# Performance work log

Hardware: AMD Instinct MI355X
Metric: run time of the kernel (lower is better)

## Reference

```python
import jax, jax.numpy as jnp
import numpy as np
import math

D_MODEL = 1024
NUM_HEADS = 16
D_K = D_MODEL // NUM_HEADS
B, L = 2, 2048
ROPE_BASE = 10000.0


def _rope_cos_sin(seq_len, dim, dtype=jnp.float32):
    inv_freq = 1.0 / (ROPE_BASE ** (jnp.arange(0, dim, 2, dtype=jnp.float32) / dim))
    t = jnp.arange(seq_len, dtype=jnp.float32)
    freqs = jnp.outer(t, inv_freq)            # [L, dim/2]
    emb = jnp.concatenate([freqs, freqs], -1)  # [L, dim]
    return jnp.cos(emb).astype(dtype), jnp.sin(emb).astype(dtype)


def _apply_rope(x, cos, sin):
    # x: [B, H, L, d_k]; cos/sin: [L, d_k]
    x1, x2 = jnp.split(x, 2, axis=-1)
    rotated = jnp.concatenate([-x2, x1], axis=-1)
    return x * cos + rotated * sin


def setup_inputs() -> dict:
    key = jax.random.key(0)
    ks = jax.random.split(key, 12)
    s = 1.0 / math.sqrt(D_MODEL)
    inp = {
        "query": jax.random.normal(ks[0], (B, L, D_MODEL), jnp.float32),
        "key":   jax.random.normal(ks[1], (B, L, D_MODEL), jnp.float32),
        "value": jax.random.normal(ks[2], (B, L, D_MODEL), jnp.float32),
        "mask":  jnp.triu(jnp.ones((L, L), jnp.bool_), k=1)[None, None],  # causal, True = masked
        "Wq": jax.random.uniform(ks[3], (D_MODEL, D_MODEL), jnp.float32, -s, s),
        "bq": jnp.zeros((D_MODEL,), jnp.float32),
        "Wk": jax.random.uniform(ks[4], (D_MODEL, D_MODEL), jnp.float32, -s, s),
        "bk": jnp.zeros((D_MODEL,), jnp.float32),
        "Wv": jax.random.uniform(ks[5], (D_MODEL, D_MODEL), jnp.float32, -s, s),
        "bv": jnp.zeros((D_MODEL,), jnp.float32),
        "Wo": jax.random.uniform(ks[6], (D_MODEL, D_MODEL), jnp.float32, -s, s),
        "bo": jnp.zeros((D_MODEL,), jnp.float32),
    }
    return inp


def reference(query, key, value, mask, Wq, bq, Wk, bk, Wv, bv, Wo, bo):
    b, l, _ = query.shape
    def proj(x, W, bias):
        return (x @ W.T + bias).reshape(b, l, NUM_HEADS, D_K).transpose(0, 2, 1, 3)
    q = proj(query, Wq, bq)   # [B, H, L, d_k]
    k = proj(key,   Wk, bk)
    v = proj(value, Wv, bv)
    cos, sin = _rope_cos_sin(l, D_K, q.dtype)
    q = _apply_rope(q, cos, sin)
    k = _apply_rope(k, cos, sin)
    scale = 1.0 / math.sqrt(D_K)
    att = jnp.einsum('bhqd,bhkd->bhqk', q, k) * scale
    att = jnp.where(mask, jnp.finfo(att.dtype).min, att)
    att = jax.nn.softmax(att, axis=-1)
    out = jnp.einsum('bhqk,bhkd->bhqd', att, v)
    out = out.transpose(0, 2, 1, 3).reshape(b, l, D_MODEL)
    return out @ Wo.T + bo
```

## Files before the change

kernel.cpp:

```cpp
#include <hip/hip_runtime.h>
#include <cstdint>

typedef _Float16 half_t;
using half8 = __attribute__((ext_vector_type(8))) half_t;
using half4 = __attribute__((ext_vector_type(4))) half_t;
using f32x4 = __attribute__((ext_vector_type(4))) float;
using f32x16 = __attribute__((ext_vector_type(16))) float;

#define LSEQ 2048
#define DM   1024
#define NH   16
#define DK   64

__device__ inline void gload_lds16(const void* g, void* l) {
    __builtin_amdgcn_global_load_lds(
        (const __attribute__((address_space(1))) uint32_t*)g,
        (__attribute__((address_space(3))) uint32_t*)l, 16, 0, 0);
}

__device__ inline uint32_t pk2(float a, float b) {
    auto h = __builtin_amdgcn_cvt_pkrtz(a, b);
    return __builtin_bit_cast(uint32_t, h);
}

__device__ inline float ex2(float x) { return __builtin_amdgcn_exp2f(x); }

__global__ __launch_bounds__(256) void cvt_kernel(
    const float* __restrict__ q, const float* __restrict__ k, const float* __restrict__ v,
    const float* __restrict__ wq, const float* __restrict__ wk,
    const float* __restrict__ wv, const float* __restrict__ wo,
    half_t* __restrict__ dst)
{
    long tid = (long)blockIdx.x * 256 + threadIdx.x;
    long e = tid * 4;
    const float* src;
    long off;
    if (e < 12582912L) {
        int a = (int)(e >> 22);
        src = (a == 0) ? q : (a == 1) ? k : v;
        off = e & 4194303L;
    } else {
        long ew = e - 12582912L;
        int w = (int)(ew >> 20);
        src = (w == 0) ? wq : (w == 1) ? wk : (w == 2) ? wv : wo;
        off = ew & 1048575L;
    }
    float4 x = *(const float4*)(src + off);
    half4 o;
    o[0] = (half_t)x.x; o[1] = (half_t)x.y; o[2] = (half_t)x.z; o[3] = (half_t)x.w;
    *(half4*)(dst + e) = o;
}

__global__ __launch_bounds__(256) void rope_tab(float* __restrict__ cosT, float* __restrict__ sinT) {
    int tid = blockIdx.x * 256 + threadIdx.x;
    int pos = tid >> 5;
    int j = tid & 31;
    float invf = powf(10000.0f, -(float)j / 32.0f);
    float a = (float)pos * invf;
    cosT[tid] = cosf(a);
    sinT[tid] = sinf(a);
}

__global__ __launch_bounds__(256) void qkv_gemm(
    const half_t* __restrict__ XH, const half_t* __restrict__ WH,
    const float* __restrict__ bq, const float* __restrict__ bk, const float* __restrict__ bv,
    half_t* __restrict__ QF, half_t* __restrict__ KF, half_t* __restrict__ VF,
    const float* __restrict__ cosT, const float* __restrict__ sinT)
{
    __shared__ alignas(16) unsigned short sA[128 * 32];
    __shared__ alignas(16) unsigned short sB[128 * 32];
    const int mode = blockIdx.z;
    const half_t* A  = XH + (long)mode * 4194304L;
    const half_t* Bw = WH + (long)mode * 1048576L;
    const float* bias = (mode == 0) ? bq : (mode == 1) ? bk : bv;

    const int tid = threadIdx.x;
    const int lane = tid & 63, wid = tid >> 6;
    const int g = lane >> 4, c = lane & 15;
    const int wr = wid >> 1, wc = wid & 1;
    const int row0 = blockIdx.y * 128, col0 = blockIdx.x * 128;

    f32x4 acc[4][4] = {};
    const int srow = lane >> 2;
    const int scol = (lane & 3) * 8;

    for (int k0 = 0; k0 < DM; k0 += 32) {
#pragma unroll
        for (int i = 0; i < 2; ++i) {
            int r = i * 64 + wid * 16;
            gload_lds16(A  + (long)(row0 + r + srow) * DM + k0 + scol, &sA[r * 32]);
            gload_lds16(Bw + (long)(col0 + r + srow) * DM + k0 + scol, &sB[r * 32]);
        }
        __syncthreads();
        half8 af[4], bf[4];
#pragma unroll
        for (int m = 0; m < 4; ++m)
            af[m] = *(const half8*)&sA[(wr * 64 + m * 16 + c) * 32 + g * 8];
#pragma unroll
        for (int n = 0; n < 4; ++n)
            bf[n] = *(const half8*)&sB[(wc * 64 + n * 16 + c) * 32 + g * 8];
#pragma unroll
        for (int m = 0; m < 4; ++m)
#pragma unroll
            for (int n = 0; n < 4; ++n)
                acc[m][n] = __builtin_amdgcn_mfma_f32_16x16x32_f16(af[m], bf[n], acc[m][n], 0, 0, 0);
        __syncthreads();
    }

    if (mode == 2) {
        const int h = blockIdx.x * 2 + wc;
#pragma unroll
        for (int n = 0; n < 4; ++n) {
            int col = col0 + wc * 64 + n * 16 + c;
            int d = n * 16 + c;
            float bvv = bias[col];
#pragma unroll
            for (int m = 0; m < 4; ++m)
#pragma unroll
                for (int r = 0; r < 4; ++r) {
                    int row = row0 + wr * 64 + m * 16 + g * 4 + r;
                    int b = row >> 11, pos = row & 2047;
                    int bh = b * NH + h;
                    long idx = (((((long)bh * 32 + (pos >> 6)) * 2 + (d >> 5)) * 4
                                 + ((pos >> 4) & 3)) * 64
                                + (((pos >> 3) & 1) * 32 + (d & 31))) * 8 + (pos & 7);
                    VF[idx] = (half_t)(acc[m][n][r] + bvv);
                }
        }
    } else {
        const float SC = (mode == 0) ? 0.125f * 1.44269504f : 1.0f;
        half_t* OF = (mode == 0) ? QF : KF;
#pragma unroll
        for (int np = 0; np < 2; ++np) {
            int col1 = col0 + wc * 64 + np * 16 + c;
            int h = col1 >> 6;
            int d1 = np * 16 + c;
            float b1 = bias[col1], b2 = bias[col1 + 32];
#pragma unroll
            for (int m = 0; m < 4; ++m)
#pragma unroll
                for (int r = 0; r < 4; ++r) {
                    int row = row0 + wr * 64 + m * 16 + g * 4 + r;
                    int b = row >> 11, pos = row & 2047;
                    int bh = b * NH + h;
                    float cv = cosT[pos * 32 + d1], sv = sinT[pos * 32 + d1];
                    float x1 = acc[m][np][r] + b1;
                    float x2 = acc[m][np + 2][r] + b2;
                    long kbase = ((long)(bh * 64 + (pos >> 5)) * 4) * 512
                               + ((c >> 3) * 32 + (pos & 31)) * 8 + (c & 7);
                    OF[kbase + (long)np * 512]       = (half_t)((x1 * cv - x2 * sv) * SC);
                    OF[kbase + (long)(np + 2) * 512] = (half_t)((x2 * cv + x1 * sv) * SC);
                }
        }
    }
}

__global__ __launch_bounds__(256) void out_gemm(
    const half_t* __restrict__ A, const half_t* __restrict__ Bw,
    const float* __restrict__ bias, float* __restrict__ o32)
{
    __shared__ alignas(16) unsigned short sA[128 * 32];
    __shared__ alignas(16) unsigned short sB[128 * 32];
    const int tid = threadIdx.x;
    const int lane = tid & 63, wid = tid >> 6;
    const int g = lane >> 4, c = lane & 15;
    const int wr = wid >> 1, wc = wid & 1;
    const int row0 = blockIdx.y * 128, col0 = blockIdx.x * 128;

    f32x4 acc[4][4] = {};
    const int srow = lane >> 2;
    const int scol = (lane & 3) * 8;

    for (int k0 = 0; k0 < DM; k0 += 32) {
#pragma unroll
        for (int i = 0; i < 2; ++i) {
            int r = i * 64 + wid * 16;
            gload_lds16(A  + (long)(row0 + r + srow) * DM + k0 + scol, &sA[r * 32]);
            gload_lds16(Bw + (long)(col0 + r + srow) * DM + k0 + scol, &sB[r * 32]);
        }
        __syncthreads();
        half8 af[4], bf[4];
#pragma unroll
        for (int m = 0; m < 4; ++m)
            af[m] = *(const half8*)&sA[(wr * 64 + m * 16 + c) * 32 + g * 8];
#pragma unroll
        for (int n = 0; n < 4; ++n)
            bf[n] = *(const half8*)&sB[(wc * 64 + n * 16 + c) * 32 + g * 8];
#pragma unroll
        for (int m = 0; m < 4; ++m)
#pragma unroll
            for (int n = 0; n < 4; ++n)
                acc[m][n] = __builtin_amdgcn_mfma_f32_16x16x32_f16(af[m], bf[n], acc[m][n], 0, 0, 0);
        __syncthreads();
    }
#pragma unroll
    for (int n = 0; n < 4; ++n) {
        int col = col0 + wc * 64 + n * 16 + c;
        float bv = bias[col];
#pragma unroll
        for (int m = 0; m < 4; ++m)
#pragma unroll
            for (int r = 0; r < 4; ++r) {
                int row = row0 + wr * 64 + m * 16 + g * 4 + r;
                o32[(long)row * DM + col] = acc[m][n][r] + bv;
            }
    }
}

__global__ __launch_bounds__(512, 2) void attn_k(
    const half_t* __restrict__ QF, const half_t* __restrict__ KF,
    const half_t* __restrict__ VF, half_t* __restrict__ AO)
{
    __shared__ half_t sK[2 * 4096];
    __shared__ half_t sV[2 * 4096];

    const int tid = threadIdx.x;
    const int lane = tid & 63, wid = tid >> 6;
    const int pr = blockIdx.x >> 5;
    const int bh = blockIdx.x & 31;
    const int qc = lane & 31, hi = lane >> 5;
    const int b = bh >> 4, h = bh & 15;
    const int lo8 = lane * 8;
    const int sub = wid & 3, grp = wid >> 2;

    const half_t* QU = QF + (long)bh * 131072;
    const half_t* KU = KF + (long)bh * 131072;
    const half_t* VU = VF + (long)bh * 131072;

    const int t1 = 15 - pr;
    const int t  = grp ? pr : t1;
    const int qb = 128 * t + 32 * sub;
    const int kend = qb + 32;
    const int kmax = 128 * t1 + 128;

    half8 qf[4];
#pragma unroll
    for (int dc = 0; dc < 4; ++dc)
        qf[dc] = *(const half8*)(QU + (qb >> 5) * 2048 + dc * 512 + lo8);

    f32x16 acc[2] = {};
    float lp[16];
#pragma unroll
    for (int r = 0; r < 16; ++r) lp[r] = 0.0f;
    float m = -INFINITY;

    union PB { uint32_t u[4]; half8 h8; };

    auto stage = [&](int buf, int k0) {
        gload_lds16(KU + (long)k0 * 64 + wid * 512 + lo8, sK + buf * 4096 + wid * 512);
        gload_lds16(VU + (long)k0 * 64 + wid * 512 + lo8, sV + buf * 4096 + wid * 512);
    };

    stage(0, 0);
    __syncthreads();

    int cur = 0;
#pragma unroll 1
    for (int k0 = 0; k0 < kmax; k0 += 64) {
        int kn = k0 + 64;
        if (kn < kmax) stage(cur ^ 1, kn);

        if (k0 < kend) {
            const half_t* bK = sK + cur * 4096;
            const half_t* bV = sV + cur * 4096;
            half8 kf0[4], kf1[4], vf[2][4];
#pragma unroll
            for (int dc = 0; dc < 4; ++dc) {
                kf0[dc] = *(const half8*)(bK + dc * 512 + lo8);
                kf1[dc] = *(const half8*)(bK + 2048 + dc * 512 + lo8);
            }
#pragma unroll
            for (int dt = 0; dt < 2; ++dt)
#pragma unroll
                for (int kc = 0; kc < 4; ++kc)
                    vf[dt][kc] = *(const half8*)(bV + (dt * 4 + kc) * 512 + lo8);

            f32x16 s0 = {}, s1 = {};
            __builtin_amdgcn_s_setprio(1);
#pragma unroll
            for (int dc = 0; dc < 4; ++dc) s0 = __builtin_amdgcn_mfma_f32_32x32x16_f16(kf0[dc], qf[dc], s0, 0, 0, 0);
#pragma unroll
            for (int dc = 0; dc < 4; ++dc) s1 = __builtin_amdgcn_mfma_f32_32x32x16_f16(kf1[dc], qf[dc], s1, 0, 0, 0);
            __builtin_amdgcn_s_setprio(0);

            if (kn >= kend) {
                int qg = qb + qc;
#pragma unroll
                for (int r = 0; r < 16; ++r) {
                    int crow = (r & 3) + 8 * (r >> 2) + 4 * hi;
                    if (k0 + crow > qg)      s0[r] = -INFINITY;
                    if (k0 + 32 + crow > qg) s1[r] = -INFINITY;
                }
            }

            float mx[8];
#pragma unroll
            for (int r = 0; r < 8; ++r)
                mx[r] = fmaxf(fmaxf(s0[r], s0[8 + r]), fmaxf(s1[r], s1[8 + r]));
#pragma unroll
            for (int st = 4; st >= 1; st >>= 1)
#pragma unroll
                for (int r = 0; r < 4; ++r)
                    if (r < st) mx[r] = fmaxf(mx[r], mx[r + st]);
            float pm = fmaxf(mx[0], __shfl_xor(mx[0], 32, 64));
            if (__any(pm > m + 8.0f)) {
                float mn = fmaxf(m, pm);
                float sc = ex2(m - mn);
#pragma unroll
                for (int r = 0; r < 16; ++r) {
                    acc[0][r] *= sc; acc[1][r] *= sc; lp[r] *= sc;
                }
                m = mn;
            }
#pragma unroll
            for (int r = 0; r < 16; ++r) {
                s0[r] = ex2(s0[r] - m);
                s1[r] = ex2(s1[r] - m);
                lp[r] += s0[r] + s1[r];
            }

            uint32_t A0[8], A1[8];
#pragma unroll
            for (int i = 0; i < 8; ++i) {
                A0[i] = pk2(s0[2 * i], s0[2 * i + 1]);
                A1[i] = pk2(s1[2 * i], s1[2 * i + 1]);
            }
            PB B00, B01, B10, B11;
            {
                auto r0 = __builtin_amdgcn_permlane32_swap(A0[0], A0[2], false, false);
                B00.u[0] = r0[0]; B00.u[2] = r0[1];
                auto r1 = __builtin_amdgcn_permlane32_swap(A0[1], A0[3], false, false);
                B00.u[1] = r1[0]; B00.u[3] = r1[1];
                auto r2 = __builtin_amdgcn_permlane32_swap(A0[4], A0[6], false, false);
                B01.u[0] = r2[0]; B01.u[2] = r2[1];
                auto r3 = __builtin_amdgcn_permlane32_swap(A0[5], A0[7], false, false);
                B01.u[1] = r3[0]; B01.u[3] = r3[1];
                auto r4 = __builtin_amdgcn_permlane32_swap(A1[0], A1[2], false, false);
                B10.u[0] = r4[0]; B10.u[2] = r4[1];
                auto r5 = __builtin_amdgcn_permlane32_swap(A1[1], A1[3], false, false);
                B10.u[1] = r5[0]; B10.u[3] = r5[1];
                auto r6 = __builtin_amdgcn_permlane32_swap(A1[4], A1[6], false, false);
                B11.u[0] = r6[0]; B11.u[2] = r6[1];
                auto r7 = __builtin_amdgcn_permlane32_swap(A1[5], A1[7], false, false);
                B11.u[1] = r7[0]; B11.u[3] = r7[1];
            }

            __builtin_amdgcn_s_setprio(1);
#pragma unroll
            for (int dt = 0; dt < 2; ++dt) {
                acc[dt] = __builtin_amdgcn_mfma_f32_32x32x16_f16(vf[dt][0], B00.h8, acc[dt], 0, 0, 0);
                acc[dt] = __builtin_amdgcn_mfma_f32_32x32x16_f16(vf[dt][1], B01.h8, acc[dt], 0, 0, 0);
                acc[dt] = __builtin_amdgcn_mfma_f32_32x32x16_f16(vf[dt][2], B10.h8, acc[dt], 0, 0, 0);
                acc[dt] = __builtin_amdgcn_mfma_f32_32x32x16_f16(vf[dt][3], B11.h8, acc[dt], 0, 0, 0);
            }
            __builtin_amdgcn_s_setprio(0);
        }
        __syncthreads();
        cur ^= 1;
    }

    float ls = lp[0];
#pragma unroll
    for (int r = 1; r < 16; ++r) ls += lp[r];
    float l = ls + __shfl_xor(ls, 32, 64);
    float inv = 1.0f / l;
    long obase = ((long)(b * LSEQ + qb + qc)) * DM + h * 64;
#pragma unroll
    for (int dt = 0; dt < 2; ++dt)
#pragma unroll
        for (int rg = 0; rg < 4; ++rg) {
            half4 o;
#pragma unroll
            for (int e = 0; e < 4; ++e) o[e] = (half_t)(acc[dt][4 * rg + e] * inv);
            *(half4*)(AO + obase + dt * 32 + 8 * rg + 4 * hi) = o;
        }
}

extern "C" void kernel_launch(void* const* d_in, const int* in_sizes, int n_in,
                              void* d_out, int out_size, void* d_ws, size_t ws_size,
                              hipStream_t stream) {
    const float* q  = (const float*)d_in[0];
    const float* k  = (const float*)d_in[1];
    const float* v  = (const float*)d_in[2];
    const float* wq = (const float*)d_in[4];
    const float* bq = (const float*)d_in[5];
    const float* wk = (const float*)d_in[6];
    const float* bk = (const float*)d_in[7];
    const float* wv = (const float*)d_in[8];
    const float* bv = (const float*)d_in[9];
    const float* wo = (const float*)d_in[10];
    const float* bo = (const float*)d_in[11];

    uint8_t* wsb = (uint8_t*)d_ws;
    half_t* XH = (half_t*)wsb;
    half_t* WH = XH + 12582912L;
    float*  COS = (float*)(wsb + 33554432L);
    float*  SIN = (float*)(wsb + 33816576L);
    half_t* QF = (half_t*)(wsb + 34078720L);
    half_t* KF = (half_t*)(wsb + 42467328L);
    half_t* VF = (half_t*)(wsb + 50855936L);
    half_t* AO = (half_t*)(wsb + 59244544L);

    cvt_kernel<<<16384, 256, 0, stream>>>(q, k, v, wq, wk, wv, wo, XH);
    rope_tab<<<256, 256, 0, stream>>>(COS, SIN);

    qkv_gemm<<<dim3(8, 32, 3), 256, 0, stream>>>(XH, WH, bq, bk, bv, QF, KF, VF, COS, SIN);

    attn_k<<<256, 512, 0, stream>>>(QF, KF, VF, AO);

    out_gemm<<<dim3(8, 32), 256, 0, stream>>>(AO, WH + 3145728L, bo, (float*)d_out);
}
```

Measured before the change: 135.3 us.

## Double-buffer GEMM LDS staging and vectorize QKV epilogue stores and rope loads

Both projection GEMMs now keep two LDS buffers and issue the next k-tile's global-to-LDS loads before computing on the current tile, so load latency can overlap MFMA work. The rope table is transposed to [dim][pos] so the QK epilogue can fetch four consecutive positions with a single float4 load. The V epilogue writes four halfs with one half4 store. The cost is double the LDS per block, which may lower occupancy, and the correctness of the single-barrier double buffer depends on how global_load_lds completion is waited on.

```diff
diff --git a/kernel.cpp b/kernel.cpp
--- a/kernel.cpp
+++ b/kernel.cpp
@@ -53,8 +53,8 @@
 
 __global__ __launch_bounds__(256) void rope_tab(float* __restrict__ cosT, float* __restrict__ sinT) {
     int tid = blockIdx.x * 256 + threadIdx.x;
-    int pos = tid >> 5;
-    int j = tid & 31;
+    int j = tid >> 11;
+    int pos = tid & 2047;
     float invf = powf(10000.0f, -(float)j / 32.0f);
     float a = (float)pos * invf;
     cosT[tid] = cosf(a);
@@ -67,8 +67,8 @@
     half_t* __restrict__ QF, half_t* __restrict__ KF, half_t* __restrict__ VF,
     const float* __restrict__ cosT, const float* __restrict__ sinT)
 {
-    __shared__ alignas(16) unsigned short sA[128 * 32];
-    __shared__ alignas(16) unsigned short sB[128 * 32];
+    __shared__ alignas(16) unsigned short sA[2][128 * 32];
+    __shared__ alignas(16) unsigned short sB[2][128 * 32];
     const int mode = blockIdx.z;
     const half_t* A  = XH + (long)mode * 4194304L;
     const half_t* Bw = WH + (long)mode * 1048576L;
@@ -84,27 +84,35 @@
     const int srow = lane >> 2;
     const int scol = (lane & 3) * 8;
 
-    for (int k0 = 0; k0 < DM; k0 += 32) {
+    auto stage = [&](int buf, int k0) {
 #pragma unroll
         for (int i = 0; i < 2; ++i) {
             int r = i * 64 + wid * 16;
-            gload_lds16(A  + (long)(row0 + r + srow) * DM + k0 + scol, &sA[r * 32]);
-            gload_lds16(Bw + (long)(col0 + r + srow) * DM + k0 + scol, &sB[r * 32]);
-        }
-        __syncthreads();
+            gload_lds16(A  + (long)(row0 + r + srow) * DM + k0 + scol, &sA[buf][r * 32]);
+            gload_lds16(Bw + (long)(col0 + r + srow) * DM + k0 + scol, &sB[buf][r * 32]);
+        }
+    };
+
+    stage(0, 0);
+    __syncthreads();
+    int cur = 0;
+#pragma unroll 1
+    for (int k0 = 0; k0 < DM; k0 += 32) {
+        if (k0 + 32 < DM) stage(cur ^ 1, k0 + 32);
         half8 af[4], bf[4];
 #pragma unroll
         for (int m = 0; m < 4; ++m)
-            af[m] = *(const half8*)&sA[(wr * 64 + m * 16 + c) * 32 + g * 8];
+            af[m] = *(const half8*)&sA[cur][(wr * 64 + m * 16 + c) * 32 + g * 8];
 #pragma unroll
         for (int n = 0; n < 4; ++n)
-            bf[n] = *(const half8*)&sB[(wc * 64 + n * 16 + c) * 32 + g * 8];
+            bf[n] = *(const half8*)&sB[cur][(wc * 64 + n * 16 + c) * 32 + g * 8];
 #pragma unroll
         for (int m = 0; m < 4; ++m)
 #pragma unroll
             for (int n = 0; n < 4; ++n)
                 acc[m][n] = __builtin_amdgcn_mfma_f32_16x16x32_f16(af[m], bf[n], acc[m][n], 0, 0, 0);
         __syncthreads();
+        cur ^= 1;
     }
 
     if (mode == 2) {
@@ -115,17 +123,18 @@
             int d = n * 16 + c;
             float bvv = bias[col];
 #pragma unroll
-            for (int m = 0; m < 4; ++m)
-#pragma unroll
-                for (int r = 0; r < 4; ++r) {
-                    int row = row0 + wr * 64 + m * 16 + g * 4 + r;
-                    int b = row >> 11, pos = row & 2047;
-                    int bh = b * NH + h;
-                    long idx = (((((long)bh * 32 + (pos >> 6)) * 2 + (d >> 5)) * 4
-                                 + ((pos >> 4) & 3)) * 64
-                                + (((pos >> 3) & 1) * 32 + (d & 31))) * 8 + (pos & 7);
-                    VF[idx] = (half_t)(acc[m][n][r] + bvv);
-                }
+            for (int m = 0; m < 4; ++m) {
+                int row = row0 + wr * 64 + m * 16 + g * 4;
+                int b = row >> 11, pos = row & 2047;
+                int bh = b * NH + h;
+                long idx = (((((long)bh * 32 + (pos >> 6)) * 2 + (d >> 5)) * 4
+                             + ((pos >> 4) & 3)) * 64
+                            + (((pos >> 3) & 1) * 32 + (d & 31))) * 8 + (pos & 7);
+                half4 o;
+#pragma unroll
+                for (int r = 0; r < 4; ++r) o[r] = (half_t)(acc[m][n][r] + bvv);
+                *(half4*)(VF + idx) = o;
+            }
         }
     } else {
         const float SC = (mode == 0) ? 0.125f * 1.44269504f : 1.0f;
@@ -136,14 +145,21 @@
             int h = col1 >> 6;
             int d1 = np * 16 + c;
             float b1 = bias[col1], b2 = bias[col1 + 32];
-#pragma unroll
-            for (int m = 0; m < 4; ++m)
+            const float* Cp = cosT + d1 * 2048;
+            const float* Sp = sinT + d1 * 2048;
+#pragma unroll
+            for (int m = 0; m < 4; ++m) {
+                int row = row0 + wr * 64 + m * 16 + g * 4;
+                int pos0 = row & 2047;
+                float4 cv4 = *(const float4*)(Cp + pos0);
+                float4 sv4 = *(const float4*)(Sp + pos0);
 #pragma unroll
                 for (int r = 0; r < 4; ++r) {
-                    int row = row0 + wr * 64 + m * 16 + g * 4 + r;
-                    int b = row >> 11, pos = row & 2047;
+                    int pos = pos0 + r;
+                    int b = (row + r) >> 11;
                     int bh = b * NH + h;
-                    float cv = cosT[pos * 32 + d1], sv = sinT[pos * 32 + d1];
+                    float cv = ((const float*)&cv4)[r];
+                    float sv = ((const float*)&sv4)[r];
                     float x1 = acc[m][np][r] + b1;
                     float x2 = acc[m][np + 2][r] + b2;
                     long kbase = ((long)(bh * 64 + (pos >> 5)) * 4) * 512
@@ -151,6 +167,7 @@
                     OF[kbase + (long)np * 512]       = (half_t)((x1 * cv - x2 * sv) * SC);
                     OF[kbase + (long)(np + 2) * 512] = (half_t)((x2 * cv + x1 * sv) * SC);
                 }
+            }
         }
     }
 }
@@ -159,8 +176,8 @@
     const half_t* __restrict__ A, const half_t* __restrict__ Bw,
     const float* __restrict__ bias, float* __restrict__ o32)
 {
-    __shared__ alignas(16) unsigned short sA[128 * 32];
-    __shared__ alignas(16) unsigned short sB[128 * 32];
+    __shared__ alignas(16) unsigned short sA[2][128 * 32];
+    __shared__ alignas(16) unsigned short sB[2][128 * 32];
     const int tid = threadIdx.x;
     const int lane = tid & 63, wid = tid >> 6;
     const int g = lane >> 4, c = lane & 15;
@@ -171,27 +188,35 @@
     const int srow = lane >> 2;
     const int scol = (lane & 3) * 8;
 
-    for (int k0 = 0; k0 < DM; k0 += 32) {
+    auto stage = [&](int buf, int k0) {
 #pragma unroll
         for (int i = 0; i < 2; ++i) {
             int r = i * 64 + wid * 16;
-            gload_lds16(A  + (long)(row0 + r + srow) * DM + k0 + scol, &sA[r * 32]);
-            gload_lds16(Bw + (long)(col0 + r + srow) * DM + k0 + scol, &sB[r * 32]);
-        }
-        __syncthreads();
+            gload_lds16(A  + (long)(row0 + r + srow) * DM + k0 + scol, &sA[buf][r * 32]);
+            gload_lds16(Bw + (long)(col0 + r + srow) * DM + k0 + scol, &sB[buf][r * 32]);
+        }
+    };
+
+    stage(0, 0);
+    __syncthreads();
+    int cur = 0;
+#pragma unroll 1
+    for (int k0 = 0; k0 < DM; k0 += 32) {
+        if (k0 + 32 < DM) stage(cur ^ 1, k0 + 32);
         half8 af[4], bf[4];
 #pragma unroll
         for (int m = 0; m < 4; ++m)
-            af[m] = *(const half8*)&sA[(wr * 64 + m * 16 + c) * 32 + g * 8];
+            af[m] = *(const half8*)&sA[cur][(wr * 64 + m * 16 + c) * 32 + g * 8];
 #pragma unroll
         for (int n = 0; n < 4; ++n)
-            bf[n] = *(const half8*)&sB[(wc * 64 + n * 16 + c) * 32 + g * 8];
+            bf[n] = *(const half8*)&sB[cur][(wc * 64 + n * 16 + c) * 32 + g * 8];
 #pragma unroll
         for (int m = 0; m < 4; ++m)
 #pragma unroll
             for (int n = 0; n < 4; ++n)
                 acc[m][n] = __builtin_amdgcn_mfma_f32_16x16x32_f16(af[m], bf[n], acc[m][n], 0, 0, 0);
         __syncthreads();
+        cur ^= 1;
     }
 #pragma unroll
     for (int n = 0; n < 4; ++n) {
```

After: 136.5 us. No clear change (+0.9%).
